# Performance work log

Measured on AMD Instinct MI355X. Metric: run time of the kernel, lower is better.

The kernel has to match this reference:

```python
import jax, jax.numpy as jnp
import numpy as np

N = 8192          # bag size (n x n attention / adjacency)
E = 262144        # number of nonzeros in sparse adjacency (avg degree 32)


def setup_inputs() -> dict:
    key = jax.random.key(0)
    k0, k1, k2, k3 = jax.random.split(key, 4)
    data_input = jax.random.normal(k0, (N, N), dtype=jnp.float32)
    edge_rows = jax.random.randint(k1, (E,), 0, N, dtype=jnp.int32)
    edge_cols = jax.random.randint(k2, (E,), 0, N, dtype=jnp.int32)
    edge_vals = jax.random.uniform(k3, (E,), dtype=jnp.float32)
    return {"data_input": data_input, "edge_rows": edge_rows,
            "edge_cols": edge_cols, "edge_vals": edge_vals}


def reference(data_input, edge_rows, edge_cols, edge_vals):
    # sparse_data_input = adj_matrix * data_input (elementwise, only on nnz)
    gathered = data_input[edge_rows, edge_cols] * edge_vals      # [E]
    # tf.sparse.reduce_sum(..., axis=1): sum nnz products per row -> [N]
    A_raw = jax.ops.segment_sum(gathered, edge_rows, num_segments=N)
    alpha = jax.nn.softmax(A_raw)                                # [N]
    return alpha, A_raw
```

## Files before the change

### kernel.cpp

```cpp
#include <hip/hip_runtime.h>
#include <math.h>

__global__ __launch_bounds__(1024)
void na_gather_agg(const float* __restrict__ data,
                   const int* __restrict__ rows,
                   const int* __restrict__ cols,
                   const float* __restrict__ vals,
                   float* __restrict__ part,
                   int E, int N) {
    __shared__ float lacc[8192];
    const int t = threadIdx.x;
    #pragma unroll
    for (int k = 0; k < 8; ++k) lacc[t + (k << 10)] = 0.0f;
    __syncthreads();

    const int e = blockIdx.x * 1024 + t;
    if (e < E) {
        const int   r = rows[e];
        const int   c = cols[e];
        const float w = vals[e];
        const float d = data[(size_t)r * (size_t)N + (size_t)c];
        atomicAdd(&lacc[r], d * w);
    }
    __syncthreads();

    float* my = part + (size_t)blockIdx.x * (size_t)N;
    #pragma unroll
    for (int k = 0; k < 8; ++k) {
        const int i = t + (k << 10);
        my[i] = lacc[i];
    }
}

__global__ __launch_bounds__(512)
void na_reduce(const float* __restrict__ part,
               float* __restrict__ A_raw,
               float* __restrict__ psum, int N) {
    const int t  = threadIdx.x;
    const int rl = t & 63;
    const int j  = t >> 6;
    const int r  = blockIdx.x * 64 + rl;

    const float* p = part + (size_t)(j * 32) * (size_t)N + r;
    float s0 = 0.f, s1 = 0.f, s2 = 0.f, s3 = 0.f;
    #pragma unroll
    for (int k = 0; k < 32; k += 4) {
        s0 += p[(size_t)(k + 0) * N];
        s1 += p[(size_t)(k + 1) * N];
        s2 += p[(size_t)(k + 2) * N];
        s3 += p[(size_t)(k + 3) * N];
    }

    __shared__ float lacc[8][64];
    lacc[j][rl] = (s0 + s1) + (s2 + s3);
    __syncthreads();

    if (t < 64) {
        float s = 0.f;
        #pragma unroll
        for (int jj = 0; jj < 8; ++jj) s += lacc[jj][rl];
        A_raw[r] = s;
        float e = expf(s);
        #pragma unroll
        for (int off = 1; off < 64; off <<= 1)
            e += __shfl_xor(e, off, 64);
        if (rl == 0) psum[blockIdx.x] = e;
    }
}

__global__ __launch_bounds__(256)
void na_normalize(const float* __restrict__ A_raw,
                  const float* __restrict__ psum,
                  float* __restrict__ alpha, int nred) {
    const int t = threadIdx.x;
    __shared__ float sinv;
    if (t < 64) {
        float v = psum[t] + psum[t + 64];
        #pragma unroll
        for (int off = 1; off < 64; off <<= 1)
            v += __shfl_xor(v, off, 64);
        if (t == 0) sinv = 1.0f / v;
    }
    __syncthreads();
    const float inv = sinv;
    const int idx = blockIdx.x * 256 + t;
    alpha[idx] = expf(A_raw[idx]) * inv;
}

extern "C" void kernel_launch(void* const* d_in, const int* in_sizes, int n_in,
                              void* d_out, int out_size, void* d_ws, size_t ws_size,
                              hipStream_t stream) {
    const float* data = (const float*)d_in[0];
    const int*   rows = (const int*)d_in[1];
    const int*   cols = (const int*)d_in[2];
    const float* vals = (const float*)d_in[3];

    const int N = out_size / 2;
    const int E = in_sizes[1];

    float* alpha = (float*)d_out;
    float* A_raw = alpha + N;
    float* part  = (float*)d_ws;
    float* psum  = part + (size_t)256 * N;

    const int nblk = (E + 1023) / 1024;

    na_gather_agg<<<dim3(nblk), dim3(1024), 0, stream>>>(
        data, rows, cols, vals, part, E, N);

    na_reduce<<<dim3(N / 64), dim3(512), 0, stream>>>(part, A_raw, psum, N);

    na_normalize<<<dim3(N / 256), dim3(256), 0, stream>>>(A_raw, psum, alpha, N / 64);
}
```

Measured before the change: 18.54 us.

## Process four edges per thread to cut partial-sum blocks from 256 to 64

Each thread now loads four edges at once with int4/float4 vector loads and does four gathers plus four LDS atomics. Because each block now covers 4096 edges, the partial buffer shrinks from 256 to 64 rows of N, so less zero-init and writeback traffic and a lighter reduce pass. It drops the bounds check and assumes E is a multiple of 4096, and each thread handles more serial atomics with fewer blocks in flight.

```diff
diff --git a/kernel.cpp b/kernel.cpp
--- a/kernel.cpp
+++ b/kernel.cpp
@@ -3,9 +3,9 @@
 
 __global__ __launch_bounds__(1024)
 void na_gather_agg(const float* __restrict__ data,
-                   const int* __restrict__ rows,
-                   const int* __restrict__ cols,
-                   const float* __restrict__ vals,
+                   const int4* __restrict__ rows4,
+                   const int4* __restrict__ cols4,
+                   const float4* __restrict__ vals4,
                    float* __restrict__ part,
                    int E, int N) {
     __shared__ float lacc[8192];
@@ -14,14 +14,19 @@
     for (int k = 0; k < 8; ++k) lacc[t + (k << 10)] = 0.0f;
     __syncthreads();
 
-    const int e = blockIdx.x * 1024 + t;
-    if (e < E) {
-        const int   r = rows[e];
-        const int   c = cols[e];
-        const float w = vals[e];
-        const float d = data[(size_t)r * (size_t)N + (size_t)c];
-        atomicAdd(&lacc[r], d * w);
-    }
+    const int q = blockIdx.x * 1024 + t;
+    const int4   r = rows4[q];
+    const int4   c = cols4[q];
+    const float4 w = vals4[q];
+    const size_t Ns = (size_t)N;
+    const float d0 = data[(size_t)r.x * Ns + (size_t)c.x];
+    const float d1 = data[(size_t)r.y * Ns + (size_t)c.y];
+    const float d2 = data[(size_t)r.z * Ns + (size_t)c.z];
+    const float d3 = data[(size_t)r.w * Ns + (size_t)c.w];
+    atomicAdd(&lacc[r.x], d0 * w.x);
+    atomicAdd(&lacc[r.y], d1 * w.y);
+    atomicAdd(&lacc[r.z], d2 * w.z);
+    atomicAdd(&lacc[r.w], d3 * w.w);
     __syncthreads();
 
     float* my = part + (size_t)blockIdx.x * (size_t)N;
@@ -41,10 +46,10 @@
     const int j  = t >> 6;
     const int r  = blockIdx.x * 64 + rl;
 
-    const float* p = part + (size_t)(j * 32) * (size_t)N + r;
+    const float* p = part + (size_t)(j * 8) * (size_t)N + r;
     float s0 = 0.f, s1 = 0.f, s2 = 0.f, s3 = 0.f;
     #pragma unroll
-    for (int k = 0; k < 32; k += 4) {
+    for (int k = 0; k < 8; k += 4) {
         s0 += p[(size_t)(k + 0) * N];
         s1 += p[(size_t)(k + 1) * N];
         s2 += p[(size_t)(k + 2) * N];
@@ -101,12 +106,13 @@
     float* alpha = (float*)d_out;
     float* A_raw = alpha + N;
     float* part  = (float*)d_ws;
-    float* psum  = part + (size_t)256 * N;
+    float* psum  = part + (size_t)64 * N;
 
-    const int nblk = (E + 1023) / 1024;
+    const int nblk = E / 4096;
 
     na_gather_agg<<<dim3(nblk), dim3(1024), 0, stream>>>(
-        data, rows, cols, vals, part, E, N);
+        data, (const int4*)rows, (const int4*)cols, (const float4*)vals,
+        part, E, N);
 
     na_reduce<<<dim3(N / 64), dim3(512), 0, stream>>>(part, A_raw, psum, N);
 
```

Result: faster. 18.12 us (-2.3%).
